# Kernel tuning notes

Measured on AMD Instinct MI355X. Metric: run time of the kernel, lower is better.

The kernel has to match this reference:

```python
import jax, jax.numpy as jnp
import numpy as np

B, S, E, H = 4, 2048, 1024, 16
D = E // H  # head_size = 64


def setup_inputs() -> dict:
    key = jax.random.key(0)
    k1, k2 = jax.random.split(key)
    x = jax.random.normal(k1, (B, S, E), dtype=jnp.float32)
    # fused QKV projection weight (torch Linear(E, 3E, bias=False))
    W_qkv = jax.random.normal(k2, (E, 3 * E), dtype=jnp.float32) * (1.0 / np.sqrt(E))
    return {"x": x, "W_qkv": W_qkv}


def reference(x, W_qkv):
    b, s, e = x.shape
    qkv = x @ W_qkv                              # [B,S,3E]
    q, k, v = jnp.split(qkv, 3, axis=-1)
    # [B,S,E] -> [B,H,S,D]
    q = q.reshape(b, s, H, D).transpose(0, 2, 1, 3)
    k = k.reshape(b, s, H, D).transpose(0, 2, 1, 3)
    v = v.reshape(b, s, H, D).transpose(0, 2, 1, 3)
    scores = jnp.einsum("bhqd,bhkd->bhqk", q, k) * (1.0 / np.sqrt(D))
    causal = jnp.tril(jnp.ones((s, s), dtype=bool))  # [S,S]
    scores = jnp.where(causal[None, None, :, :], scores, jnp.float32(-jnp.inf))
    attn = jax.nn.softmax(scores, axis=-1)
    # dropout is identity in eval mode (p effectively 0 for this baseline)
    out = jnp.einsum("bhqk,bhkd->bhqd", attn, v)  # [B,H,S,D]
    out = out.transpose(0, 2, 1, 3).reshape(b, s, e)
    # NOTE: original forward never applies output_projection; faithful omission.
    return out
```

## Files before the change

### kernel.cpp

```cpp
#include <hip/hip_runtime.h>
#include <hip/hip_bf16.h>
#include <cstdint>
#include <cstddef>

#define GLOBAL_AS __attribute__((address_space(1)))
#define LDS_AS __attribute__((address_space(3)))

typedef short bf16x8 __attribute__((ext_vector_type(8)));
typedef float f32x4 __attribute__((ext_vector_type(4)));

constexpr int Bq = 4, Sq = 2048, Eq = 1024, Hh = 16;
constexpr int M = Bq * Sq;
constexpr int K = 1024;
constexpr int N = 3 * Eq;

#define SMSC 0.18033688f
#define SMBIAS (-16.0f)

#if __has_builtin(__builtin_amdgcn_exp2f)
#define EXP2F(x) __builtin_amdgcn_exp2f(x)
#else
#define EXP2F(x) exp2f(x)
#endif

static __device__ __forceinline__ unsigned f2bf(float f) {
    union { float f; unsigned u; } v; v.f = f;
    unsigned r = v.u + 0x7fffu + ((v.u >> 16) & 1u);
    return r >> 16;
}

static __device__ __forceinline__ unsigned pk2(float a, float b) {
    union { __hip_bfloat162 h; unsigned u; } c;
    c.h = __float22bfloat162_rn(float2{a, b});
    return c.u;
}

static __device__ __forceinline__ void pl32swap(unsigned& a, unsigned& b) {
    asm("v_permlane32_swap_b32 %0, %1" : "+v"(a), "+v"(b));
}
static __device__ __forceinline__ void pl16swap(unsigned& a, unsigned& b) {
    asm("v_permlane16_swap_b32 %0, %1" : "+v"(a), "+v"(b));
}

__global__ __launch_bounds__(256) void prep(const float* __restrict__ X,
                                            unsigned short* __restrict__ Xb,
                                            const float* __restrict__ W,
                                            unsigned short* __restrict__ Wt) {
    __shared__ unsigned short tile[64 * 72];
    const int t = threadIdx.x;
    const int bx = blockIdx.x;
    if (bx < 4096) {
        size_t i = ((size_t)bx * 256 + t) * 8;
        float4 a = *reinterpret_cast<const float4*>(X + i);
        float4 b = *reinterpret_cast<const float4*>(X + i + 4);
        uint4 o;
        o.x = pk2(a.x, a.y);
        o.y = pk2(a.z, a.w);
        o.z = pk2(b.x, b.y);
        o.w = pk2(b.z, b.w);
        *reinterpret_cast<uint4*>(Xb + i) = o;
        return;
    }
    const int idx = bx - 4096;
    const int n0 = (idx % 48) * 64;
    const int k0 = (idx / 48) * 64;
    #pragma unroll
    for (int p = 0; p < 4; ++p) {
        int c = p * 256 + t;
        int row = c >> 4;
        int c4 = (c & 15) * 4;
        float4 v = *reinterpret_cast<const float4*>(W + (size_t)(k0 + row) * N + n0 + c4);
        *reinterpret_cast<unsigned*>(&tile[row * 72 + c4]) = pk2(v.x, v.y);
        *reinterpret_cast<unsigned*>(&tile[row * 72 + c4 + 2]) = pk2(v.z, v.w);
    }
    __syncthreads();
    #pragma unroll
    for (int p = 0; p < 2; ++p) {
        int c = t + p * 256;
        int n = c & 63;
        int kc = (c >> 6) * 8;
        unsigned v[8];
        #pragma unroll
        for (int j = 0; j < 8; ++j) v[j] = tile[(kc + j) * 72 + n];
        uint4 o;
        o.x = v[0] | (v[1] << 16);
        o.y = v[2] | (v[3] << 16);
        o.z = v[4] | (v[5] << 16);
        o.w = v[6] | (v[7] << 16);
        *reinterpret_cast<uint4*>(Wt + (size_t)(n0 + n) * K + k0 + kc) = o;
    }
}

__global__ __launch_bounds__(256) void gemm_qkv(const unsigned short* __restrict__ A,
                                                const unsigned short* __restrict__ Bt,
                                                unsigned short* __restrict__ C,
                                                unsigned short* __restrict__ Vt) {
    __shared__ unsigned short Alds[128 * 64];
    __shared__ unsigned short Blds[128 * 64];
    const int t = threadIdx.x;
    const int lane = t & 63, w = t >> 6;
    const int wm = w >> 1, wn = w & 1;
    const int m0 = blockIdx.y * 128, n0 = blockIdx.x * 128;
    const int lr = lane & 15, quad = lane >> 4;
    const int sw = lr & 7;

    f32x4 acc[4][4] = {};
    for (int k0 = 0; k0 < K; k0 += 64) {
        #pragma unroll
        for (int p = 0; p < 4; ++p) {
            int c = p * 256 + t;
            int row = c >> 3;
            int lch = (c & 7) ^ (row & 7);
            const unsigned short* ga = A + (size_t)(m0 + row) * K + k0 + lch * 8;
            __builtin_amdgcn_global_load_lds((const GLOBAL_AS unsigned int*)ga,
                                             (LDS_AS unsigned int*)&Alds[c * 8], 16, 0, 0);
            const unsigned short* gb = Bt + (size_t)(n0 + row) * K + k0 + lch * 8;
            __builtin_amdgcn_global_load_lds((const GLOBAL_AS unsigned int*)gb,
                                             (LDS_AS unsigned int*)&Blds[c * 8], 16, 0, 0);
        }
        __syncthreads();
        #pragma unroll
        for (int ks = 0; ks < 2; ++ks) {
            bf16x8 af[4], bfr[4];
            const int pch = ((ks * 4 + quad) ^ sw) << 3;
            #pragma unroll
            for (int mt = 0; mt < 4; ++mt)
                af[mt] = *reinterpret_cast<const bf16x8*>(
                    &Alds[(wm * 64 + mt * 16 + lr) * 64 + pch]);
            #pragma unroll
            for (int nt = 0; nt < 4; ++nt)
                bfr[nt] = *reinterpret_cast<const bf16x8*>(
                    &Blds[(wn * 64 + nt * 16 + lr) * 64 + pch]);
            #pragma unroll
            for (int mt = 0; mt < 4; ++mt)
                #pragma unroll
                for (int nt = 0; nt < 4; ++nt)
                    acc[mt][nt] = __builtin_amdgcn_mfma_f32_16x16x32_bf16(af[mt], bfr[nt],
                                                                          acc[mt][nt], 0, 0, 0);
        }
        __syncthreads();
    }
    if (n0 < 2 * Eq) {
        #pragma unroll
        for (int mt = 0; mt < 4; ++mt)
            #pragma unroll
            for (int nt = 0; nt < 4; ++nt)
                #pragma unroll
                for (int r = 0; r < 4; ++r) {
                    int row = m0 + wm * 64 + mt * 16 + quad * 4 + r;
                    int col = n0 + wn * 64 + nt * 16 + lr;
                    C[(size_t)row * N + col] = (unsigned short)f2bf(acc[mt][nt][r]);
                }
    } else {
        const int b2 = m0 >> 11;
        const int sbase = (m0 & 2047) + wm * 64;
        #pragma unroll
        for (int mt = 0; mt < 4; ++mt)
            #pragma unroll
            for (int nt = 0; nt < 4; ++nt) {
                int hd = n0 - 2 * Eq + wn * 64 + nt * 16 + lr;
                size_t rowV = (size_t)(b2 * Hh + (hd >> 6)) * 64 + (hd & 63);
                int s = sbase + mt * 16 + quad * 4;
                uint2 val;
                val.x = f2bf(acc[mt][nt][0]) | (f2bf(acc[mt][nt][1]) << 16);
                val.y = f2bf(acc[mt][nt][2]) | (f2bf(acc[mt][nt][3]) << 16);
                *reinterpret_cast<uint2*>(Vt + rowV * Sq + s) = val;
            }
    }
}

__global__ __launch_bounds__(256, 4) void flash_attn(const unsigned short* __restrict__ QKV,
                                                     const unsigned short* __restrict__ Vt,
                                                     float* __restrict__ Out) {
    __shared__ unsigned short Klds[2][32 * 64];
    __shared__ unsigned short Vlds[2][64 * 32];
    const int t = threadIdx.x;
    const int lane = t & 63, w = t >> 6;
    const int lr = lane & 15, quad = lane >> 4;
    const int hb = blockIdx.x;
    const int h = hb & 15, b = hb >> 4;
    const int y = (int)blockIdx.y;
    const int sw = lr & 7;

    const unsigned short* Kbase = QKV + (size_t)b * Sq * N + Eq + h * 64;
    const unsigned short* Vbase = Vt + (size_t)((b * Hh + h) * 64) * Sq;

    bf16x8 ones;
    #pragma unroll
    for (int z = 0; z < 8; ++z) ones[z] = (short)0x3F80;

    auto stage = [&](int j, int buf) {
        const int kv0 = j * 32;
        {
            int row = t >> 3;
            int lch = (t & 7) ^ (row & 7);
            const unsigned short* gk = Kbase + (size_t)(kv0 + row) * N + lch * 8;
            __builtin_amdgcn_global_load_lds((const GLOBAL_AS unsigned int*)gk,
                                             (LDS_AS unsigned int*)&Klds[buf][t * 8], 16, 0, 0);
        }
        {
            int row = t >> 2;
            int ch = t & 3;
            const unsigned short* gv = Vbase + (size_t)row * Sq + kv0 + ch * 8;
            __builtin_amdgcn_global_load_lds((const GLOBAL_AS unsigned int*)gv,
                                             (LDS_AS unsigned int*)&Vlds[buf][t * 8], 16, 0, 0);
        }
    };

    #pragma unroll 1
    for (int pass = 0; pass < 2; ++pass) {
        const int i = pass ? y : (15 - y);
        const int jmax = 4 * i + 3;
        const int jd = 4 * i + w;
        const int qbase = i * 128 + w * 32;

        bf16x8 qf[2][2];
        #pragma unroll
        for (int mt = 0; mt < 2; ++mt)
            #pragma unroll
            for (int ks = 0; ks < 2; ++ks)
                qf[mt][ks] = *reinterpret_cast<const bf16x8*>(
                    QKV + (size_t)(b * Sq + qbase + mt * 16 + lr) * N + h * 64 + ks * 32 + quad * 8);

        f32x4 o[2][4] = {};
        f32x4 lsum[2] = {};

        stage(0, 0);
        int cur = 0;
        for (int j = 0; j <= jmax; ++j) {
            __syncthreads();
            if (j < jmax) stage(j + 1, cur ^ 1);

            if (j <= jd) {
                const unsigned short* Kb = Klds[cur];
                const unsigned short* Vb = Vlds[cur];
                const int kv0 = j * 32;

                f32x4 sa[2][2] = {};
                #pragma unroll
                for (int ks = 0; ks < 2; ++ks) {
                    const int pch = ((ks * 4 + quad) ^ sw) << 3;
                    #pragma unroll
                    for (int kt = 0; kt < 2; ++kt) {
                        bf16x8 kf = *reinterpret_cast<const bf16x8*>(&Kb[(kt * 16 + lr) * 64 + pch]);
                        #pragma unroll
                        for (int qt = 0; qt < 2; ++qt)
                            sa[kt][qt] = __builtin_amdgcn_mfma_f32_16x16x32_bf16(kf, qf[qt][ks],
                                                                                 sa[kt][qt], 0, 0, 0);
                    }
                }

                float p[2][2][4];
                if (j == jd) {
                    #pragma unroll
                    for (int kt = 0; kt < 2; ++kt)
                        #pragma unroll
                        for (int qt = 0; qt < 2; ++qt)
                            #pragma unroll
                            for (int r = 0; r < 4; ++r) {
                                int kvg = kv0 + kt * 16 + quad * 4 + r;
                                int qg = qbase + qt * 16 + lr;
                                float sc = fmaf(sa[kt][qt][r], SMSC, SMBIAS);
                                sc = (kvg > qg) ? -1e30f : sc;
                                p[kt][qt][r] = EXP2F(sc);
                            }
                } else {
                    #pragma unroll
                    for (int kt = 0; kt < 2; ++kt)
                        #pragma unroll
                        for (int qt = 0; qt < 2; ++qt)
                            #pragma unroll
                            for (int r = 0; r < 4; ++r)
                                p[kt][qt][r] = EXP2F(fmaf(sa[kt][qt][r], SMSC, SMBIAS));
                }

                bf16x8 af[2];
                #pragma unroll
                for (int qt = 0; qt < 2; ++qt) {
                    unsigned w00 = pk2(p[0][qt][0], p[0][qt][1]);
                    unsigned w01 = pk2(p[0][qt][2], p[0][qt][3]);
                    unsigned w10 = pk2(p[1][qt][0], p[1][qt][1]);
                    unsigned w11 = pk2(p[1][qt][2], p[1][qt][3]);
                    pl32swap(w00, w10); pl16swap(w00, w10);
                    pl32swap(w01, w11); pl16swap(w01, w11);
                    union { unsigned u[4]; bf16x8 v; } pa;
                    pa.u[0] = w00; pa.u[1] = w01; pa.u[2] = w10; pa.u[3] = w11;
                    af[qt] = pa.v;
                }

                #pragma unroll
                for (int dt = 0; dt < 4; ++dt) {
                    bf16x8 vf = *reinterpret_cast<const bf16x8*>(&Vb[(dt * 16 + lr) * 32 + quad * 8]);
                    #pragma unroll
                    for (int qt = 0; qt < 2; ++qt)
                        o[qt][dt] = __builtin_amdgcn_mfma_f32_16x16x32_bf16(af[qt], vf,
                                                                            o[qt][dt], 0, 0, 0);
                }
                #pragma unroll
                for (int qt = 0; qt < 2; ++qt)
                    lsum[qt] = __builtin_amdgcn_mfma_f32_16x16x32_bf16(af[qt], ones,
                                                                       lsum[qt], 0, 0, 0);
            }
            cur ^= 1;
        }

        #pragma unroll
        for (int mt = 0; mt < 2; ++mt)
            #pragma unroll
            for (int r = 0; r < 4; ++r) {
                float inv = 1.0f / lsum[mt][r];
                int qg = qbase + mt * 16 + quad * 4 + r;
                #pragma unroll
                for (int dt = 0; dt < 4; ++dt)
                    Out[(size_t)(b * Sq + qg) * Eq + h * 64 + dt * 16 + lr] = o[mt][dt][r] * inv;
            }
    }
}

extern "C" void kernel_launch(void* const* d_in, const int* in_sizes, int n_in,
                              void* d_out, int out_size, void* d_ws, size_t ws_size,
                              hipStream_t stream) {
    const float* x  = (const float*)d_in[0];
    const float* Wq = (const float*)d_in[1];
    float* out = (float*)d_out;

    unsigned short* xb  = (unsigned short*)d_ws;
    unsigned short* qkv = xb + (size_t)M * K;
    unsigned short* Wt  = qkv + (size_t)M * N;
    unsigned short* Vt  = Wt + (size_t)N * K;

    prep<<<dim3(4096 + 768), 256, 0, stream>>>(x, xb, Wq, Wt);
    gemm_qkv<<<dim3(N / 128, M / 128), 256, 0, stream>>>(xb, Wt, qkv, Vt);
    flash_attn<<<dim3(Hh * Bq, 8), 256, 0, stream>>>(qkv, Vt, out);
}
```

Measured before the change: 219.3 us.

## Split flash-attention blocks into two-wave halves to cut causal idle work

Each 4-wave attention block is split into two 2-wave blocks covering the lower and upper query halves of a 128-row tile, doubling the grid. The lower half stops its KV loop earlier, so waves no longer sit idle at barriers while other waves finish diagonal tiles. This removes wasted causal iterations and raises block count. The cost is K/V tiles loaded twice per 128-query tile, more global traffic, and fewer threads to share each staging step.

```diff
diff --git a/kernel.cpp b/kernel.cpp
--- a/kernel.cpp
+++ b/kernel.cpp
@@ -169,17 +169,19 @@
     }
 }
 
-__global__ __launch_bounds__(256, 4) void flash_attn(const unsigned short* __restrict__ QKV,
+__global__ __launch_bounds__(128, 4) void flash_attn(const unsigned short* __restrict__ QKV,
                                                      const unsigned short* __restrict__ Vt,
                                                      float* __restrict__ Out) {
     __shared__ unsigned short Klds[2][32 * 64];
     __shared__ unsigned short Vlds[2][64 * 32];
     const int t = threadIdx.x;
-    const int lane = t & 63, w = t >> 6;
+    const int lane = t & 63, wl = t >> 6;
     const int lr = lane & 15, quad = lane >> 4;
     const int hb = blockIdx.x;
     const int h = hb & 15, b = hb >> 4;
-    const int y = (int)blockIdx.y;
+    const int y2 = (int)blockIdx.y;
+    const int y = y2 >> 1;
+    const int half = y2 & 1;
     const int sw = lr & 7;
 
     const unsigned short* Kbase = QKV + (size_t)b * Sq * N + Eq + h * 64;
@@ -191,26 +193,31 @@
 
     auto stage = [&](int j, int buf) {
         const int kv0 = j * 32;
-        {
-            int row = t >> 3;
-            int lch = (t & 7) ^ (row & 7);
+        #pragma unroll
+        for (int p = 0; p < 2; ++p) {
+            int c = p * 128 + t;
+            int row = c >> 3;
+            int lch = (c & 7) ^ (row & 7);
             const unsigned short* gk = Kbase + (size_t)(kv0 + row) * N + lch * 8;
             __builtin_amdgcn_global_load_lds((const GLOBAL_AS unsigned int*)gk,
-                                             (LDS_AS unsigned int*)&Klds[buf][t * 8], 16, 0, 0);
-        }
-        {
-            int row = t >> 2;
-            int ch = t & 3;
+                                             (LDS_AS unsigned int*)&Klds[buf][c * 8], 16, 0, 0);
+        }
+        #pragma unroll
+        for (int p = 0; p < 2; ++p) {
+            int c = p * 128 + t;
+            int row = c >> 2;
+            int ch = c & 3;
             const unsigned short* gv = Vbase + (size_t)row * Sq + kv0 + ch * 8;
             __builtin_amdgcn_global_load_lds((const GLOBAL_AS unsigned int*)gv,
-                                             (LDS_AS unsigned int*)&Vlds[buf][t * 8], 16, 0, 0);
+                                             (LDS_AS unsigned int*)&Vlds[buf][c * 8], 16, 0, 0);
         }
     };
 
     #pragma unroll 1
     for (int pass = 0; pass < 2; ++pass) {
         const int i = pass ? y : (15 - y);
-        const int jmax = 4 * i + 3;
+        const int w = half * 2 + wl;
+        const int jmaxl = 4 * i + half * 2 + 1;
         const int jd = 4 * i + w;
         const int qbase = i * 128 + w * 32;
 
@@ -227,9 +234,9 @@
 
         stage(0, 0);
         int cur = 0;
-        for (int j = 0; j <= jmax; ++j) {
+        for (int j = 0; j <= jmaxl; ++j) {
             __syncthreads();
-            if (j < jmax) stage(j + 1, cur ^ 1);
+            if (j < jmaxl) stage(j + 1, cur ^ 1);
 
             if (j <= jd) {
                 const unsigned short* Kb = Klds[cur];
@@ -331,5 +338,5 @@
 
     prep<<<dim3(4096 + 768), 256, 0, stream>>>(x, xb, Wq, Wt);
     gemm_qkv<<<dim3(N / 128, M / 128), 256, 0, stream>>>(xb, Wt, qkv, Vt);
-    flash_attn<<<dim3(Hh * Bq, 8), 256, 0, stream>>>(qkv, Vt, out);
-}
+    flash_attn<<<dim3(Hh * Bq, 16), 128, 0, stream>>>(qkv, Vt, out);
+}
```

Measured after the change: 236.0 us. 1.08x slower.
